# Optimization experiments

Measured on AMD Instinct MI355X. Metric: run time of the kernel, lower is better.

The kernel has to match this reference:

```python
import jax, jax.numpy as jnp
import numpy as np

TAU, LBDA, THETA = 0.25, 0.15, 0.3
N_WARPS, N_ITERS = 5, 5
EPS = 1e-12  # GRAD_IS_ZERO


def centered_gradient(x):
    # centered [-0.5,0,0.5] stencil with one-sided boundaries (matches conv+boundary-fix)
    dx = jnp.concatenate([0.5 * (x[..., 1:2] - x[..., 0:1]),
                          0.5 * (x[..., 2:] - x[..., :-2]),
                          0.5 * (x[..., -1:] - x[..., -2:-1])], axis=-1)
    dy = jnp.concatenate([0.5 * (x[:, :, 1:2] - x[:, :, 0:1]),
                          0.5 * (x[:, :, 2:] - x[:, :, :-2]),
                          0.5 * (x[:, :, -1:] - x[:, :, -2:-1])], axis=2)
    return dx, dy


def forward_gradient(x):
    # [-1,1] forward difference, zero at last col/row (conv 'same' + zeroed last slice)
    dx = jnp.concatenate([x[..., 1:] - x[..., :-1], jnp.zeros_like(x[..., :1])], axis=-1)
    dy = jnp.concatenate([x[:, :, 1:] - x[:, :, :-1], jnp.zeros_like(x[:, :, :1])], axis=2)
    return dx, dy


def forward_divergence(px, py):
    # backward difference with zero left/top boundary; last entry = -p[-2]
    dx = jnp.concatenate([px[..., :1], px[..., 1:-1] - px[..., :-2], -px[..., -2:-1]], axis=-1)
    dy = jnp.concatenate([py[:, :, :1], py[:, :, 1:-1] - py[:, :, :-2], -py[:, :, -2:-1]], axis=2)
    return dx + dy


def warp_image(im, u, v):
    # bilinear warp by pixel flow (u,v); grid math mirrors the STN spatial_transformer:
    # normalized identity grid in [-1,1] plus flow*2/size, mapped back via (g+1)*size/2,
    # with indices clipped to the image (border behavior).
    B, C, H, W = im.shape
    dt = im.dtype
    gx = jnp.linspace(-1.0, 1.0, W, dtype=dt)[None, None, None, :]
    gy = jnp.linspace(-1.0, 1.0, H, dtype=dt)[None, None, :, None]
    x = (gx + u * (2.0 / W) + 1.0) * (W / 2.0)
    y = (gy + v * (2.0 / H) + 1.0) * (H / 2.0)
    x0 = jnp.floor(x).astype(jnp.int32)
    y0 = jnp.floor(y).astype(jnp.int32)
    x0i = jnp.clip(x0, 0, W - 1); x1i = jnp.clip(x0 + 1, 0, W - 1)
    y0i = jnp.clip(y0, 0, H - 1); y1i = jnp.clip(y0 + 1, 0, H - 1)
    x0f = x0i.astype(dt); x1f = x1i.astype(dt)
    y0f = y0i.astype(dt); y1f = y1i.astype(dt)
    flat = im.reshape(B, H * W)

    def gather(yi, xi):
        idx = (yi * W + xi).reshape(B, H * W)
        return jnp.take_along_axis(flat, idx, axis=1).reshape(B, C, H, W)

    Ia = gather(y0i, x0i); Ib = gather(y1i, x0i)
    Ic = gather(y0i, x1i); Id = gather(y1i, x1i)
    wa = (x1f - x) * (y1f - y); wb = (x1f - x) * (y - y0f)
    wc = (x - x0f) * (y1f - y); wd = (x - x0f) * (y - y0f)
    return wa * Ia + wb * Ib + wc * Ic + wd * Id


def tv_l1_scale(x1, x2, u1, u2):
    l_t = LBDA * THETA
    taut = TAU / THETA
    d2x, d2y = centered_gradient(x2)
    z = jnp.zeros_like(x1)
    p11, p12, p21, p22 = z, z, z, z
    rho = z
    for _ in range(N_WARPS):
        x2w = warp_image(x2, u1, u2)
        dxw = warp_image(d2x, u1, u2)
        dyw = warp_image(d2y, u1, u2)
        grad = dxw * dxw + dyw * dyw + EPS
        rho_c = x2w - dxw * u1 - dyw * u2 - x1
        for _ in range(N_ITERS):
            rho = rho_c + dxw * u1 + dyw * u2 + EPS
            m1 = rho < -l_t * grad
            m2 = rho > l_t * grad
            m3 = (~m1) & (~m2) & (grad > EPS)
            s = jnp.where(m1, l_t, jnp.where(m2, -l_t, jnp.where(m3, -rho / grad, 0.0)))
            v1 = s * dxw + u1
            v2 = s * dyw + u2
            u1 = v1 + THETA * forward_divergence(p11, p12)
            u2 = v2 + THETA * forward_divergence(p21, p22)
            u1x, u1y = forward_gradient(u1)
            u2x, u2y = forward_gradient(u2)
            n1 = 1.0 + taut * jnp.sqrt(u1x * u1x + u1y * u1y + EPS)
            n2 = 1.0 + taut * jnp.sqrt(u2x * u2x + u2y * u2y + EPS)
            p11 = (p11 + taut * u1x) / n1
            p12 = (p12 + taut * u1y) / n1
            p21 = (p21 + taut * u2x) / n2
            p22 = (p22 + taut * u2y) / n2
    return u1, u2, rho


def setup_inputs() -> dict:
    key = jax.random.key(0)
    k1, k2 = jax.random.split(key)
    B, H, W = 8, 480, 480
    x1 = jax.random.uniform(k1, (B, 1, H, W), dtype=jnp.float32)
    x2 = jax.random.uniform(k2, (B, 1, H, W), dtype=jnp.float32)
    u1 = jnp.zeros((B, 1, H, W), dtype=jnp.float32)
    u2 = jnp.zeros((B, 1, H, W), dtype=jnp.float32)
    return {"x1": x1, "x2": x2, "u1": u1, "u2": u2}


def reference(x1, x2, u1, u2):
    return tv_l1_scale(x1, x2, u1, u2)
```

## Files before the change

### kernel.cpp

```cpp
#include <hip/hip_runtime.h>

#pragma clang fp contract(off)


constexpr int B = 8, H = 480, W = 480;
constexpr int HW = H * W;
constexpr int N = B * HW;

constexpr float THETA = (float)0.3;
constexpr float L_T  = (float)(0.15 * 0.3);
constexpr float TAUT = (float)(0.25 / 0.3);
constexpr float EPSF = (float)1e-12;

#define RW 42
#define RH 40
#define HALO 5
#define TW 32
#define TH 30
#define NTX 15
#define NTY 16
#define TPB 512
#define NPX 4
#define RPX (RW*RH)

template <int WARPK>
__global__ __launch_bounds__(TPB, 4) void k_fused(
    const float* __restrict__ x1, const float* __restrict__ x2,
    const float* __restrict__ u1In, const float* __restrict__ u2In,
    const float2* __restrict__ uIn, const float4* __restrict__ pIn,
    float* __restrict__ u1Out, float* __restrict__ u2Out,
    float2* __restrict__ uOut, float4* __restrict__ pOut,
    float* __restrict__ rhoOut)
{
  __shared__ float2 su[RPX];
  __shared__ float2 spA[RPX];
  __shared__ float2 spB[RPX];

  int blk = blockIdx.x;
  int bx = blk % NTX;
  int by = (blk / NTX) % NTY;
  int b  = blk / (NTX * NTY);
  const int ox = bx * TW - HALO;
  const int oy = by * TH - HALO;
  const int tid = threadIdx.x;
  const int base = b * HW;
  const float* __restrict__ im = x2 + base;

  float cdx[NPX], cdy[NPX], crc[NPX];

#pragma unroll
  for (int k = 0; k < NPX; ++k) {
    int idx = tid + k * TPB;
    if (idx < RPX) {
      int ly = idx / RW, lx = idx - ly * RW;
      int px = ox + lx, py = oy + ly;
      bool valid = (px >= 0 && px < W && py >= 0 && py < H);
      if (valid) {
        int gi = base + py * W + px;
        float u, v;
        if (WARPK == 0) { u = u1In[gi]; v = u2In[gi]; }
        else            { float2 uv = uIn[gi]; u = uv.x; v = uv.y; }
        const float step = 2.0f / 479.0f;
        float gx = -1.0f + (float)px * step;
        float gy = -1.0f + (float)py * step;
        float X = ((gx + u * (float)(2.0 / 480.0)) + 1.0f) * 240.0f;
        float Y = ((gy + v * (float)(2.0 / 480.0)) + 1.0f) * 240.0f;
        float fX = floorf(X), fY = floorf(Y);
        int ix = (int)fX, iy = (int)fY;
        int x0i = min(max(ix, 0), W - 1);
        int x1i = min(max(ix + 1, 0), W - 1);
        int y0i = min(max(iy, 0), H - 1);
        int y1i = min(max(iy + 1, 0), H - 1);
        float x0f = (float)x0i, x1f = (float)x1i;
        float y0f = (float)y0i, y1f = (float)y1i;
        float wa = (x1f - X) * (y1f - Y);
        float wb = (x1f - X) * (Y - y0f);
        float wc = (X - x0f) * (y1f - Y);
        float wd = (X - x0f) * (Y - y0f);
        int xmA = max(x0i - 1, 0), xpA = min(x0i + 1, W - 1);
        int xmB = max(x1i - 1, 0), xpB = min(x1i + 1, W - 1);
        int ymA = max(y0i - 1, 0), ypA = min(y0i + 1, H - 1);
        int ymB = max(y1i - 1, 0), ypB = min(y1i + 1, H - 1);
        int y0W = y0i * W, y1W = y1i * W;
        int ymAW = ymA * W, ypAW = ypA * W, ymBW = ymB * W, ypBW = ypB * W;
        float Ia = im[y0W + x0i], Ib = im[y1W + x0i];
        float Ic = im[y0W + x1i], Id = im[y1W + x1i];
        float dA = 0.5f * (im[y0W + xpA] - im[y0W + xmA]);
        float dB = 0.5f * (im[y1W + xpA] - im[y1W + xmA]);
        float dC = 0.5f * (im[y0W + xpB] - im[y0W + xmB]);
        float dD = 0.5f * (im[y1W + xpB] - im[y1W + xmB]);
        float eA = 0.5f * (im[ypAW + x0i] - im[ymAW + x0i]);
        float eB = 0.5f * (im[ypBW + x0i] - im[ymBW + x0i]);
        float eC = 0.5f * (im[ypAW + x1i] - im[ymAW + x1i]);
        float eD = 0.5f * (im[ypBW + x1i] - im[ymBW + x1i]);
        float x2w = ((wa * Ia + wb * Ib) + wc * Ic) + wd * Id;
        float dxw = ((wa * dA + wb * dB) + wc * dC) + wd * dD;
        float dyw = ((wa * eA + wb * eB) + wc * eC) + wd * eD;
        cdx[k] = dxw; cdy[k] = dyw;
        crc[k] = ((x2w - dxw * u) - dyw * v) - x1[gi];
        float4 q;
        if (WARPK == 0) q = make_float4(0.f, 0.f, 0.f, 0.f);
        else            q = pIn[gi];
        su[idx]  = make_float2(u, v);
        spA[idx] = make_float2(q.x, q.z);
        spB[idx] = make_float2(q.y, q.w);
      }
    }
  }
  __syncthreads();

  for (int t = 1; t <= 5; ++t) {
    int ulox = ox + t; if (ulox < 0) ulox = 0;
    int uloy = oy + t; if (uloy < 0) uloy = 0;
    int uhix = (ox + RW >= W) ? W : (ox + RW + 1 - t);
    int uhiy = (oy + RH >= H) ? H : (oy + RH + 1 - t);

#pragma unroll
    for (int k = 0; k < NPX; ++k) {
      int idx = tid + k * TPB;
      if (idx < RPX) {
        int ly = idx / RW, lx = idx - ly * RW;
        int px = ox + lx, py = oy + ly;
        if (px >= ulox && px < uhix && py >= uloy && py < uhiy) {
          float2 uo  = su[idx];
          float2 pAo = spA[idx];
          float2 pBo = spB[idx];
          float2 pl = spA[idx - 1];
          float2 pu = spB[idx - RW];
          float dx = cdx[k], dy = cdy[k];
          float u = uo.x, v = uo.y;
          float rho = ((crc[k] + dx * u) + dy * v) + EPSF;
          float grad = (dx * dx + dy * dy) + EPSF;
          float lt_g = L_T * grad;
          float s;
          if (rho < -lt_g)      s = L_T;
          else if (rho > lt_g)  s = -L_T;
          else if (grad > EPSF) s = (-rho) / grad;
          else                  s = 0.f;
          float v1 = s * dx + u;
          float v2 = s * dy + v;
          float dvx1, dvy1, dvx2, dvy2;
          if (px == 0)          dvx1 = pAo.x;
          else if (px == W - 1) dvx1 = -pl.x;
          else                  dvx1 = pAo.x - pl.x;
          if (py == 0)          dvy1 = pBo.x;
          else if (py == H - 1) dvy1 = -pu.x;
          else                  dvy1 = pBo.x - pu.x;
          if (px == 0)          dvx2 = pAo.y;
          else if (px == W - 1) dvx2 = -pl.y;
          else                  dvx2 = pAo.y - pl.y;
          if (py == 0)          dvy2 = pBo.y;
          else if (py == H - 1) dvy2 = -pu.y;
          else                  dvy2 = pBo.y - pu.y;
          float nu1 = v1 + THETA * (dvx1 + dvy1);
          float nu2 = v2 + THETA * (dvx2 + dvy2);
          su[idx] = make_float2(nu1, nu2);
          if (WARPK == 2 && t == 5) {
            if (lx >= HALO && lx < HALO + TW && ly >= HALO && ly < HALO + TH)
              rhoOut[base + py * W + px] = rho;
          }
        }
      }
    }
    __syncthreads();

    if (!(WARPK == 2 && t == 5)) {
      int phix = (ox + RW >= W) ? W : (ox + RW - t);
      int phiy = (oy + RH >= H) ? H : (oy + RH - t);
#pragma unroll
      for (int k = 0; k < NPX; ++k) {
        int idx = tid + k * TPB;
        if (idx < RPX) {
          int ly = idx / RW, lx = idx - ly * RW;
          int px = ox + lx, py = oy + ly;
          if (px >= ulox && px < phix && py >= uloy && py < phiy) {
            float2 uo = su[idx];
            float2 uR = su[idx + 1];
            float2 uD = su[idx + RW];
            float2 pAo = spA[idx];
            float2 pBo = spB[idx];
            float u1c = uo.x, u2c = uo.y;
            float u1x = (px < W - 1) ? uR.x - u1c : 0.f;
            float u1y = (py < H - 1) ? uD.x - u1c : 0.f;
            float u2x = (px < W - 1) ? uR.y - u2c : 0.f;
            float u2y = (py < H - 1) ? uD.y - u2c : 0.f;
            float n1 = 1.0f + TAUT * sqrtf((u1x * u1x + u1y * u1y) + EPSF);
            float n2 = 1.0f + TAUT * sqrtf((u2x * u2x + u2y * u2y) + EPSF);
            float np11 = (pAo.x + TAUT * u1x) / n1;
            float np12 = (pBo.x + TAUT * u1y) / n1;
            float np21 = (pAo.y + TAUT * u2x) / n2;
            float np22 = (pBo.y + TAUT * u2y) / n2;
            spA[idx] = make_float2(np11, np21);
            spB[idx] = make_float2(np12, np22);
          }
        }
      }
    }
    __syncthreads();
  }

#pragma unroll
  for (int k = 0; k < NPX; ++k) {
    int idx = tid + k * TPB;
    if (idx < RPX) {
      int ly = idx / RW, lx = idx - ly * RW;
      if (lx >= HALO && lx < HALO + TW && ly >= HALO && ly < HALO + TH) {
        int gi = base + (oy + ly) * W + (ox + lx);
        float2 uo = su[idx];
        if (WARPK == 2) {
          u1Out[gi] = uo.x;
          u2Out[gi] = uo.y;
        } else {
          uOut[gi] = uo;
          float2 a = spA[idx], c = spB[idx];
          pOut[gi] = make_float4(a.x, c.x, a.y, c.y);
        }
      }
    }
  }
}

extern "C" void kernel_launch(void* const* d_in, const int* in_sizes, int n_in,
                              void* d_out, int out_size, void* d_ws, size_t ws_size,
                              hipStream_t stream) {
  const float* x1 = (const float*)d_in[0];
  const float* x2 = (const float*)d_in[1];
  const float* u1_in = (const float*)d_in[2];
  const float* u2_in = (const float*)d_in[3];

  float* u1o  = (float*)d_out;
  float* u2o  = u1o + (size_t)N;
  float* rhoo = u1o + (size_t)2 * N;

  float* ws  = (float*)d_ws;
  float2* uA = (float2*)ws;
  float4* pA = (float4*)(ws + (size_t)2 * N);
  float2* uB = (float2*)(ws + (size_t)6 * N);
  float4* pB = (float4*)(ws + (size_t)8 * N);

  dim3 grd(NTX * NTY * B), blk(TPB);
  k_fused<0><<<grd, blk, 0, stream>>>(x1, x2, u1_in, u2_in, nullptr, nullptr,
                                      nullptr, nullptr, uA, pA, rhoo);
  k_fused<1><<<grd, blk, 0, stream>>>(x1, x2, nullptr, nullptr, uA, pA,
                                      nullptr, nullptr, uB, pB, rhoo);
  k_fused<1><<<grd, blk, 0, stream>>>(x1, x2, nullptr, nullptr, uB, pB,
                                      nullptr, nullptr, uA, pA, rhoo);
  k_fused<1><<<grd, blk, 0, stream>>>(x1, x2, nullptr, nullptr, uA, pA,
                                      nullptr, nullptr, uB, pB, rhoo);
  k_fused<2><<<grd, blk, 0, stream>>>(x1, x2, nullptr, nullptr, uB, pB,
                                      u1o, u2o, nullptr, nullptr, rhoo);
}
```

Baseline: 367.4 us.

## Keep per-pixel state in registers with vertical strips per thread and wider tiles

Each thread now owns a vertical strip of four pixels in one column and keeps u, p, and the warp coefficients in registers across the five inner iterations. Shared memory is used only for neighbours across strip boundaries, which cuts LDS traffic and drops the per-pixel index divisions. Per-pixel iteration limits are precomputed, and the precomputed grad and lambda*grad values are cached. The tile grows from 32 to 40 columns, which lowers the halo recompute ratio but raises register pressure and leaves 12 of 512 threads idle.

```diff
diff --git a/kernel.cpp b/kernel.cpp
--- a/kernel.cpp
+++ b/kernel.cpp
@@ -12,16 +12,16 @@
 constexpr float TAUT = (float)(0.25 / 0.3);
 constexpr float EPSF = (float)1e-12;
 
-#define RW 42
+#define RW 50
 #define RH 40
 #define HALO 5
-#define TW 32
+#define TW 40
 #define TH 30
-#define NTX 15
+#define NTX 12
 #define NTY 16
 #define TPB 512
-#define NPX 4
-#define RPX (RW*RH)
+#define NSTRIP 500
+#define SJ 4
 
 template <int WARPK>
 __global__ __launch_bounds__(TPB, 4) void k_fused(
@@ -32,188 +32,192 @@
     float2* __restrict__ uOut, float4* __restrict__ pOut,
     float* __restrict__ rhoOut)
 {
-  __shared__ float2 su[RPX];
-  __shared__ float2 spA[RPX];
-  __shared__ float2 spB[RPX];
-
-  int blk = blockIdx.x;
-  int bx = blk % NTX;
-  int by = (blk / NTX) % NTY;
-  int b  = blk / (NTX * NTY);
+  __shared__ float2 su[RW * RH];
+  __shared__ float2 spA[RW * RH];
+  __shared__ float2 spB[RW * RH];
+
+  const int blk = blockIdx.x;
+  const int bx = blk % NTX;
+  const int by = (blk / NTX) % NTY;
+  const int b  = blk / (NTX * NTY);
   const int ox = bx * TW - HALO;
   const int oy = by * TH - HALO;
   const int tid = threadIdx.x;
+  const bool ok = (tid < NSTRIP);
+  const int c  = tid % RW;
+  const int rs = tid / RW;
+  const int pxc = ox + c;
+  const int pyb = oy + rs * SJ;
+  const int idxb = rs * SJ * RW + c;
+  const bool bL = (pxc == 0), bR = (pxc == W - 1);
   const int base = b * HW;
   const float* __restrict__ im = x2 + base;
 
-  float cdx[NPX], cdy[NPX], crc[NPX];
-
-#pragma unroll
-  for (int k = 0; k < NPX; ++k) {
-    int idx = tid + k * TPB;
-    if (idx < RPX) {
-      int ly = idx / RW, lx = idx - ly * RW;
-      int px = ox + lx, py = oy + ly;
-      bool valid = (px >= 0 && px < W && py >= 0 && py < H);
-      if (valid) {
-        int gi = base + py * W + px;
-        float u, v;
-        if (WARPK == 0) { u = u1In[gi]; v = u2In[gi]; }
-        else            { float2 uv = uIn[gi]; u = uv.x; v = uv.y; }
-        const float step = 2.0f / 479.0f;
-        float gx = -1.0f + (float)px * step;
-        float gy = -1.0f + (float)py * step;
-        float X = ((gx + u * (float)(2.0 / 480.0)) + 1.0f) * 240.0f;
-        float Y = ((gy + v * (float)(2.0 / 480.0)) + 1.0f) * 240.0f;
-        float fX = floorf(X), fY = floorf(Y);
-        int ix = (int)fX, iy = (int)fY;
-        int x0i = min(max(ix, 0), W - 1);
-        int x1i = min(max(ix + 1, 0), W - 1);
-        int y0i = min(max(iy, 0), H - 1);
-        int y1i = min(max(iy + 1, 0), H - 1);
-        float x0f = (float)x0i, x1f = (float)x1i;
-        float y0f = (float)y0i, y1f = (float)y1i;
-        float wa = (x1f - X) * (y1f - Y);
-        float wb = (x1f - X) * (Y - y0f);
-        float wc = (X - x0f) * (y1f - Y);
-        float wd = (X - x0f) * (Y - y0f);
-        int xmA = max(x0i - 1, 0), xpA = min(x0i + 1, W - 1);
-        int xmB = max(x1i - 1, 0), xpB = min(x1i + 1, W - 1);
-        int ymA = max(y0i - 1, 0), ypA = min(y0i + 1, H - 1);
-        int ymB = max(y1i - 1, 0), ypB = min(y1i + 1, H - 1);
-        int y0W = y0i * W, y1W = y1i * W;
-        int ymAW = ymA * W, ypAW = ypA * W, ymBW = ymB * W, ypBW = ypB * W;
-        float Ia = im[y0W + x0i], Ib = im[y1W + x0i];
-        float Ic = im[y0W + x1i], Id = im[y1W + x1i];
-        float dA = 0.5f * (im[y0W + xpA] - im[y0W + xmA]);
-        float dB = 0.5f * (im[y1W + xpA] - im[y1W + xmA]);
-        float dC = 0.5f * (im[y0W + xpB] - im[y0W + xmB]);
-        float dD = 0.5f * (im[y1W + xpB] - im[y1W + xmB]);
-        float eA = 0.5f * (im[ypAW + x0i] - im[ymAW + x0i]);
-        float eB = 0.5f * (im[ypBW + x0i] - im[ymBW + x0i]);
-        float eC = 0.5f * (im[ypAW + x1i] - im[ymAW + x1i]);
-        float eD = 0.5f * (im[ypBW + x1i] - im[ymBW + x1i]);
-        float x2w = ((wa * Ia + wb * Ib) + wc * Ic) + wd * Id;
-        float dxw = ((wa * dA + wb * dB) + wc * dC) + wd * dD;
-        float dyw = ((wa * eA + wb * eB) + wc * eC) + wd * eD;
-        cdx[k] = dxw; cdy[k] = dyw;
-        crc[k] = ((x2w - dxw * u) - dyw * v) - x1[gi];
-        float4 q;
-        if (WARPK == 0) q = make_float4(0.f, 0.f, 0.f, 0.f);
-        else            q = pIn[gi];
-        su[idx]  = make_float2(u, v);
-        spA[idx] = make_float2(q.x, q.z);
-        spB[idx] = make_float2(q.y, q.w);
-      }
+  float ru1[SJ], ru2[SJ];
+  float rp11[SJ], rp12[SJ], rp21[SJ], rp22[SJ];
+  float cdx[SJ], cdy[SJ], crc[SJ];
+  float grd[SJ], ltg[SJ];
+  int   tu[SJ], tp[SJ];
+
+#pragma unroll
+  for (int j = 0; j < SJ; ++j) {
+    const int py = pyb + j;
+    const bool valid = ok && (pxc >= 0) && (pxc < W) && (py >= 0) && (py < H);
+    if (valid) {
+      int Lx = max(pxc - ox, -ox);
+      int Ly = max(py - oy, -oy);
+      int Rxu = (ox + RW >= W) ? 99 : (ox + RW - pxc);
+      int Ryu = (oy + RH >= H) ? 99 : (oy + RH - py);
+      tu[j] = min(min(Lx, Ly), min(Rxu, Ryu));
+      int Rxp = (ox + RW >= W) ? 99 : (ox + RW - 1 - pxc);
+      int Ryp = (oy + RH >= H) ? 99 : (oy + RH - 1 - py);
+      tp[j] = min(min(Lx, Ly), min(Rxp, Ryp));
+    } else { tu[j] = 0; tp[j] = 0; }
+    if (valid) {
+      const int gi = base + py * W + pxc;
+      float u, v;
+      if (WARPK == 0) { u = u1In[gi]; v = u2In[gi]; }
+      else            { float2 uv = uIn[gi]; u = uv.x; v = uv.y; }
+      const float step = 2.0f / 479.0f;
+      float gx = -1.0f + (float)pxc * step;
+      float gy = -1.0f + (float)py * step;
+      float X = ((gx + u * (float)(2.0 / 480.0)) + 1.0f) * 240.0f;
+      float Y = ((gy + v * (float)(2.0 / 480.0)) + 1.0f) * 240.0f;
+      float fX = floorf(X), fY = floorf(Y);
+      int ix = (int)fX, iy = (int)fY;
+      int x0i = min(max(ix, 0), W - 1);
+      int x1i = min(max(ix + 1, 0), W - 1);
+      int y0i = min(max(iy, 0), H - 1);
+      int y1i = min(max(iy + 1, 0), H - 1);
+      float x0f = (float)x0i, x1f = (float)x1i;
+      float y0f = (float)y0i, y1f = (float)y1i;
+      float wa = (x1f - X) * (y1f - Y);
+      float wb = (x1f - X) * (Y - y0f);
+      float wc = (X - x0f) * (y1f - Y);
+      float wd = (X - x0f) * (Y - y0f);
+      int xmA = max(x0i - 1, 0), xpA = min(x0i + 1, W - 1);
+      int xmB = max(x1i - 1, 0), xpB = min(x1i + 1, W - 1);
+      int ymA = max(y0i - 1, 0), ypA = min(y0i + 1, H - 1);
+      int ymB = max(y1i - 1, 0), ypB = min(y1i + 1, H - 1);
+      int y0W = y0i * W, y1W = y1i * W;
+      int ymAW = ymA * W, ypAW = ypA * W, ymBW = ymB * W, ypBW = ypB * W;
+      float Ia = im[y0W + x0i], Ib = im[y1W + x0i];
+      float Ic = im[y0W + x1i], Id = im[y1W + x1i];
+      float dA = 0.5f * (im[y0W + xpA] - im[y0W + xmA]);
+      float dB = 0.5f * (im[y1W + xpA] - im[y1W + xmA]);
+      float dC = 0.5f * (im[y0W + xpB] - im[y0W + xmB]);
+      float dD = 0.5f * (im[y1W + xpB] - im[y1W + xmB]);
+      float eA = 0.5f * (im[ypAW + x0i] - im[ymAW + x0i]);
+      float eB = 0.5f * (im[ypBW + x0i] - im[ymBW + x0i]);
+      float eC = 0.5f * (im[ypAW + x1i] - im[ymAW + x1i]);
+      float eD = 0.5f * (im[ypBW + x1i] - im[ymBW + x1i]);
+      float x2w = ((wa * Ia + wb * Ib) + wc * Ic) + wd * Id;
+      float dxw = ((wa * dA + wb * dB) + wc * dC) + wd * dD;
+      float dyw = ((wa * eA + wb * eB) + wc * eC) + wd * eD;
+      cdx[j] = dxw; cdy[j] = dyw;
+      crc[j] = ((x2w - dxw * u) - dyw * v) - x1[gi];
+      grd[j] = (dxw * dxw + dyw * dyw) + EPSF;
+      ltg[j] = L_T * grd[j];
+      ru1[j] = u; ru2[j] = v;
+      float4 q;
+      if (WARPK == 0) q = make_float4(0.f, 0.f, 0.f, 0.f);
+      else            q = pIn[gi];
+      rp11[j] = q.x; rp12[j] = q.y; rp21[j] = q.z; rp22[j] = q.w;
+      const int idx = idxb + j * RW;
+      spA[idx] = make_float2(q.x, q.z);
+      spB[idx] = make_float2(q.y, q.w);
     }
   }
   __syncthreads();
 
   for (int t = 1; t <= 5; ++t) {
-    int ulox = ox + t; if (ulox < 0) ulox = 0;
-    int uloy = oy + t; if (uloy < 0) uloy = 0;
-    int uhix = (ox + RW >= W) ? W : (ox + RW + 1 - t);
-    int uhiy = (oy + RH >= H) ? H : (oy + RH + 1 - t);
-
-#pragma unroll
-    for (int k = 0; k < NPX; ++k) {
-      int idx = tid + k * TPB;
-      if (idx < RPX) {
-        int ly = idx / RW, lx = idx - ly * RW;
-        int px = ox + lx, py = oy + ly;
-        if (px >= ulox && px < uhix && py >= uloy && py < uhiy) {
-          float2 uo  = su[idx];
-          float2 pAo = spA[idx];
-          float2 pBo = spB[idx];
-          float2 pl = spA[idx - 1];
-          float2 pu = spB[idx - RW];
-          float dx = cdx[k], dy = cdy[k];
-          float u = uo.x, v = uo.y;
-          float rho = ((crc[k] + dx * u) + dy * v) + EPSF;
-          float grad = (dx * dx + dy * dy) + EPSF;
-          float lt_g = L_T * grad;
-          float s;
-          if (rho < -lt_g)      s = L_T;
-          else if (rho > lt_g)  s = -L_T;
-          else if (grad > EPSF) s = (-rho) / grad;
-          else                  s = 0.f;
-          float v1 = s * dx + u;
-          float v2 = s * dy + v;
-          float dvx1, dvy1, dvx2, dvy2;
-          if (px == 0)          dvx1 = pAo.x;
-          else if (px == W - 1) dvx1 = -pl.x;
-          else                  dvx1 = pAo.x - pl.x;
-          if (py == 0)          dvy1 = pBo.x;
-          else if (py == H - 1) dvy1 = -pu.x;
-          else                  dvy1 = pBo.x - pu.x;
-          if (px == 0)          dvx2 = pAo.y;
-          else if (px == W - 1) dvx2 = -pl.y;
-          else                  dvx2 = pAo.y - pl.y;
-          if (py == 0)          dvy2 = pBo.y;
-          else if (py == H - 1) dvy2 = -pu.y;
-          else                  dvy2 = pBo.y - pu.y;
-          float nu1 = v1 + THETA * (dvx1 + dvy1);
-          float nu2 = v2 + THETA * (dvx2 + dvy2);
-          su[idx] = make_float2(nu1, nu2);
-          if (WARPK == 2 && t == 5) {
-            if (lx >= HALO && lx < HALO + TW && ly >= HALO && ly < HALO + TH)
-              rhoOut[base + py * W + px] = rho;
-          }
+#pragma unroll
+    for (int j = 0; j < SJ; ++j) {
+      if (t <= tu[j]) {
+        const int idx = idxb + j * RW;
+        const int py = pyb + j;
+        float dx = cdx[j], dy = cdy[j];
+        float u = ru1[j], v = ru2[j];
+        float rho = ((crc[j] + dx * u) + dy * v) + EPSF;
+        float s;
+        if (rho < -ltg[j])      s = L_T;
+        else if (rho > ltg[j])  s = -L_T;
+        else if (grd[j] > EPSF) s = (-rho) / grd[j];
+        else                    s = 0.f;
+        float v1 = s * dx + u;
+        float v2 = s * dy + v;
+        float2 pl = spA[idx - 1];
+        float pu12, pu22;
+        if (j == 0) { float2 q = spB[idx - RW]; pu12 = q.x; pu22 = q.y; }
+        else        { pu12 = rp12[j - 1];       pu22 = rp22[j - 1]; }
+        float dvx1, dvy1, dvx2, dvy2;
+        if (bL)               dvx1 = rp11[j];
+        else if (bR)          dvx1 = -pl.x;
+        else                  dvx1 = rp11[j] - pl.x;
+        if (py == 0)          dvy1 = rp12[j];
+        else if (py == H - 1) dvy1 = -pu12;
+        else                  dvy1 = rp12[j] - pu12;
+        if (bL)               dvx2 = rp21[j];
+        else if (bR)          dvx2 = -pl.y;
+        else                  dvx2 = rp21[j] - pl.y;
+        if (py == 0)          dvy2 = rp22[j];
+        else if (py == H - 1) dvy2 = -pu22;
+        else                  dvy2 = rp22[j] - pu22;
+        float nu1 = v1 + THETA * (dvx1 + dvy1);
+        float nu2 = v2 + THETA * (dvx2 + dvy2);
+        ru1[j] = nu1; ru2[j] = nu2;
+        if (!(WARPK == 2 && t == 5)) su[idx] = make_float2(nu1, nu2);
+        if (WARPK == 2 && t == 5) {
+          int ly = rs * SJ + j;
+          if (c >= HALO && c < HALO + TW && ly >= HALO && ly < HALO + TH)
+            rhoOut[base + py * W + pxc] = rho;
         }
       }
     }
     __syncthreads();
 
     if (!(WARPK == 2 && t == 5)) {
-      int phix = (ox + RW >= W) ? W : (ox + RW - t);
-      int phiy = (oy + RH >= H) ? H : (oy + RH - t);
-#pragma unroll
-      for (int k = 0; k < NPX; ++k) {
-        int idx = tid + k * TPB;
-        if (idx < RPX) {
-          int ly = idx / RW, lx = idx - ly * RW;
-          int px = ox + lx, py = oy + ly;
-          if (px >= ulox && px < phix && py >= uloy && py < phiy) {
-            float2 uo = su[idx];
-            float2 uR = su[idx + 1];
-            float2 uD = su[idx + RW];
-            float2 pAo = spA[idx];
-            float2 pBo = spB[idx];
-            float u1c = uo.x, u2c = uo.y;
-            float u1x = (px < W - 1) ? uR.x - u1c : 0.f;
-            float u1y = (py < H - 1) ? uD.x - u1c : 0.f;
-            float u2x = (px < W - 1) ? uR.y - u2c : 0.f;
-            float u2y = (py < H - 1) ? uD.y - u2c : 0.f;
-            float n1 = 1.0f + TAUT * sqrtf((u1x * u1x + u1y * u1y) + EPSF);
-            float n2 = 1.0f + TAUT * sqrtf((u2x * u2x + u2y * u2y) + EPSF);
-            float np11 = (pAo.x + TAUT * u1x) / n1;
-            float np12 = (pBo.x + TAUT * u1y) / n1;
-            float np21 = (pAo.y + TAUT * u2x) / n2;
-            float np22 = (pBo.y + TAUT * u2y) / n2;
-            spA[idx] = make_float2(np11, np21);
-            spB[idx] = make_float2(np12, np22);
-          }
+#pragma unroll
+      for (int j = 0; j < SJ; ++j) {
+        if (t <= tp[j]) {
+          const int idx = idxb + j * RW;
+          const int py = pyb + j;
+          float u1c = ru1[j], u2c = ru2[j];
+          float2 uR = su[idx + 1];
+          float uD1, uD2;
+          if (j < SJ - 1) { uD1 = ru1[j + 1]; uD2 = ru2[j + 1]; }
+          else            { float2 q = su[idx + RW]; uD1 = q.x; uD2 = q.y; }
+          float u1x = (pxc < W - 1) ? uR.x - u1c : 0.f;
+          float u1y = (py  < H - 1) ? uD1  - u1c : 0.f;
+          float u2x = (pxc < W - 1) ? uR.y - u2c : 0.f;
+          float u2y = (py  < H - 1) ? uD2  - u2c : 0.f;
+          float n1 = 1.0f + TAUT * sqrtf((u1x * u1x + u1y * u1y) + EPSF);
+          float n2 = 1.0f + TAUT * sqrtf((u2x * u2x + u2y * u2y) + EPSF);
+          float np11 = (rp11[j] + TAUT * u1x) / n1;
+          float np12 = (rp12[j] + TAUT * u1y) / n1;
+          float np21 = (rp21[j] + TAUT * u2x) / n2;
+          float np22 = (rp22[j] + TAUT * u2y) / n2;
+          rp11[j] = np11; rp12[j] = np12; rp21[j] = np21; rp22[j] = np22;
+          spA[idx] = make_float2(np11, np21);
+          if (j == SJ - 1) spB[idx] = make_float2(np12, np22);
         }
       }
-    }
-    __syncthreads();
+      __syncthreads();
+    }
   }
 
-#pragma unroll
-  for (int k = 0; k < NPX; ++k) {
-    int idx = tid + k * TPB;
-    if (idx < RPX) {
-      int ly = idx / RW, lx = idx - ly * RW;
-      if (lx >= HALO && lx < HALO + TW && ly >= HALO && ly < HALO + TH) {
-        int gi = base + (oy + ly) * W + (ox + lx);
-        float2 uo = su[idx];
+  if (ok && c >= HALO && c < HALO + TW) {
+#pragma unroll
+    for (int j = 0; j < SJ; ++j) {
+      int ly = rs * SJ + j;
+      if (ly >= HALO && ly < HALO + TH) {
+        int gi = base + (pyb + j) * W + pxc;
         if (WARPK == 2) {
-          u1Out[gi] = uo.x;
-          u2Out[gi] = uo.y;
+          u1Out[gi] = ru1[j];
+          u2Out[gi] = ru2[j];
         } else {
-          uOut[gi] = uo;
-          float2 a = spA[idx], c = spB[idx];
-          pOut[gi] = make_float4(a.x, c.x, a.y, c.y);
+          uOut[gi] = make_float2(ru1[j], ru2[j]);
+          pOut[gi] = make_float4(rp11[j], rp12[j], rp21[j], rp22[j]);
         }
       }
     }
```

New measurement: 373.9 us. Within noise of the previous version (+1.8%).

## Widen spatial tiles and hoist per-pixel iteration bounds into registers

Applied to the files above, without the earlier changes.

Widens the tile from 32 to 40 columns, so the 5-pixel halo is a smaller share of each block's work while the same 4 pixels-per-thread slots are kept. Each pixel's index math, the number of valid u/p update steps, the output mask, and the grad and lambda-theta-grad terms are computed once before the iteration loop, so the loop no longer recomputes bounds each step. It also removes the trailing barriers after the last step. The cost is more live registers under a 512x4 launch bound, and more shared memory per block, which may cut the number of resident blocks.

```diff
diff --git a/kernel.cpp b/kernel.cpp
--- a/kernel.cpp
+++ b/kernel.cpp
@@ -12,12 +12,12 @@
 constexpr float TAUT = (float)(0.25 / 0.3);
 constexpr float EPSF = (float)1e-12;
 
-#define RW 42
+#define RW 50
 #define RH 40
 #define HALO 5
-#define TW 32
+#define TW 40
 #define TH 30
-#define NTX 15
+#define NTX 12
 #define NTY 16
 #define TPB 512
 #define NPX 4
@@ -36,10 +36,10 @@
   __shared__ float2 spA[RPX];
   __shared__ float2 spB[RPX];
 
-  int blk = blockIdx.x;
-  int bx = blk % NTX;
-  int by = (blk / NTX) % NTY;
-  int b  = blk / (NTX * NTY);
+  const int blk = blockIdx.x;
+  const int bx = blk % NTX;
+  const int by = (blk / NTX) % NTY;
+  const int b  = blk / (NTX * NTY);
   const int ox = bx * TW - HALO;
   const int oy = by * TH - HALO;
   const int tid = threadIdx.x;
@@ -47,174 +47,171 @@
   const float* __restrict__ im = x2 + base;
 
   float cdx[NPX], cdy[NPX], crc[NPX];
+  float grd[NPX], ltg[NPX];
+  int   idxA[NPX], pxA[NPX], pyA[NPX], giA[NPX];
+  int   tu[NPX], tp[NPX];
+  bool  wout[NPX];
 
 #pragma unroll
   for (int k = 0; k < NPX; ++k) {
-    int idx = tid + k * TPB;
-    if (idx < RPX) {
-      int ly = idx / RW, lx = idx - ly * RW;
-      int px = ox + lx, py = oy + ly;
-      bool valid = (px >= 0 && px < W && py >= 0 && py < H);
-      if (valid) {
-        int gi = base + py * W + px;
-        float u, v;
-        if (WARPK == 0) { u = u1In[gi]; v = u2In[gi]; }
-        else            { float2 uv = uIn[gi]; u = uv.x; v = uv.y; }
-        const float step = 2.0f / 479.0f;
-        float gx = -1.0f + (float)px * step;
-        float gy = -1.0f + (float)py * step;
-        float X = ((gx + u * (float)(2.0 / 480.0)) + 1.0f) * 240.0f;
-        float Y = ((gy + v * (float)(2.0 / 480.0)) + 1.0f) * 240.0f;
-        float fX = floorf(X), fY = floorf(Y);
-        int ix = (int)fX, iy = (int)fY;
-        int x0i = min(max(ix, 0), W - 1);
-        int x1i = min(max(ix + 1, 0), W - 1);
-        int y0i = min(max(iy, 0), H - 1);
-        int y1i = min(max(iy + 1, 0), H - 1);
-        float x0f = (float)x0i, x1f = (float)x1i;
-        float y0f = (float)y0i, y1f = (float)y1i;
-        float wa = (x1f - X) * (y1f - Y);
-        float wb = (x1f - X) * (Y - y0f);
-        float wc = (X - x0f) * (y1f - Y);
-        float wd = (X - x0f) * (Y - y0f);
-        int xmA = max(x0i - 1, 0), xpA = min(x0i + 1, W - 1);
-        int xmB = max(x1i - 1, 0), xpB = min(x1i + 1, W - 1);
-        int ymA = max(y0i - 1, 0), ypA = min(y0i + 1, H - 1);
-        int ymB = max(y1i - 1, 0), ypB = min(y1i + 1, H - 1);
-        int y0W = y0i * W, y1W = y1i * W;
-        int ymAW = ymA * W, ypAW = ypA * W, ymBW = ymB * W, ypBW = ypB * W;
-        float Ia = im[y0W + x0i], Ib = im[y1W + x0i];
-        float Ic = im[y0W + x1i], Id = im[y1W + x1i];
-        float dA = 0.5f * (im[y0W + xpA] - im[y0W + xmA]);
-        float dB = 0.5f * (im[y1W + xpA] - im[y1W + xmA]);
-        float dC = 0.5f * (im[y0W + xpB] - im[y0W + xmB]);
-        float dD = 0.5f * (im[y1W + xpB] - im[y1W + xmB]);
-        float eA = 0.5f * (im[ypAW + x0i] - im[ymAW + x0i]);
-        float eB = 0.5f * (im[ypBW + x0i] - im[ymBW + x0i]);
-        float eC = 0.5f * (im[ypAW + x1i] - im[ymAW + x1i]);
-        float eD = 0.5f * (im[ypBW + x1i] - im[ymBW + x1i]);
-        float x2w = ((wa * Ia + wb * Ib) + wc * Ic) + wd * Id;
-        float dxw = ((wa * dA + wb * dB) + wc * dC) + wd * dD;
-        float dyw = ((wa * eA + wb * eB) + wc * eC) + wd * eD;
-        cdx[k] = dxw; cdy[k] = dyw;
-        crc[k] = ((x2w - dxw * u) - dyw * v) - x1[gi];
-        float4 q;
-        if (WARPK == 0) q = make_float4(0.f, 0.f, 0.f, 0.f);
-        else            q = pIn[gi];
-        su[idx]  = make_float2(u, v);
-        spA[idx] = make_float2(q.x, q.z);
-        spB[idx] = make_float2(q.y, q.w);
+    const int idx = tid + k * TPB;
+    idxA[k] = idx;
+    const int ly = idx / RW, lx = idx - ly * RW;
+    const int px = ox + lx, py = oy + ly;
+    pxA[k] = px; pyA[k] = py;
+    giA[k] = base + py * W + px;
+    const bool inreg = (idx < RPX);
+    const bool valid = inreg && (px >= 0) && (px < W) && (py >= 0) && (py < H);
+    wout[k] = inreg && lx >= HALO && lx < HALO + TW &&
+              ly >= HALO && ly < HALO + TH;
+    if (valid) {
+      int Lx = max(px - ox, -ox);
+      int Ly = max(py - oy, -oy);
+      int Rxu = (ox + RW >= W) ? 99 : (ox + RW - px);
+      int Ryu = (oy + RH >= H) ? 99 : (oy + RH - py);
+      tu[k] = min(min(Lx, Ly), min(Rxu, Ryu));
+      int Rxp = (ox + RW >= W) ? 99 : (ox + RW - 1 - px);
+      int Ryp = (oy + RH >= H) ? 99 : (oy + RH - 1 - py);
+      tp[k] = min(min(Lx, Ly), min(Rxp, Ryp));
+
+      const int gi = giA[k];
+      float u, v;
+      if (WARPK == 0) { u = u1In[gi]; v = u2In[gi]; }
+      else            { float2 uv = uIn[gi]; u = uv.x; v = uv.y; }
+      const float step = 2.0f / 479.0f;
+      float gx = -1.0f + (float)px * step;
+      float gy = -1.0f + (float)py * step;
+      float X = ((gx + u * (float)(2.0 / 480.0)) + 1.0f) * 240.0f;
+      float Y = ((gy + v * (float)(2.0 / 480.0)) + 1.0f) * 240.0f;
+      float fX = floorf(X), fY = floorf(Y);
+      int ix = (int)fX, iy = (int)fY;
+      int x0i = min(max(ix, 0), W - 1);
+      int x1i = min(max(ix + 1, 0), W - 1);
+      int y0i = min(max(iy, 0), H - 1);
+      int y1i = min(max(iy + 1, 0), H - 1);
+      float x0f = (float)x0i, x1f = (float)x1i;
+      float y0f = (float)y0i, y1f = (float)y1i;
+      float wa = (x1f - X) * (y1f - Y);
+      float wb = (x1f - X) * (Y - y0f);
+      float wc = (X - x0f) * (y1f - Y);
+      float wd = (X - x0f) * (Y - y0f);
+      int xmA = max(x0i - 1, 0), xpA = min(x0i + 1, W - 1);
+      int xmB = max(x1i - 1, 0), xpB = min(x1i + 1, W - 1);
+      int ymA = max(y0i - 1, 0), ypA = min(y0i + 1, H - 1);
+      int ymB = max(y1i - 1, 0), ypB = min(y1i + 1, H - 1);
+      int y0W = y0i * W, y1W = y1i * W;
+      int ymAW = ymA * W, ypAW = ypA * W, ymBW = ymB * W, ypBW = ypB * W;
+      float Ia = im[y0W + x0i], Ib = im[y1W + x0i];
+      float Ic = im[y0W + x1i], Id = im[y1W + x1i];
+      float dA = 0.5f * (im[y0W + xpA] - im[y0W + xmA]);
+      float dB = 0.5f * (im[y1W + xpA] - im[y1W + xmA]);
+      float dC = 0.5f * (im[y0W + xpB] - im[y0W + xmB]);
+      float dD = 0.5f * (im[y1W + xpB] - im[y1W + xmB]);
+      float eA = 0.5f * (im[ypAW + x0i] - im[ymAW + x0i]);
+      float eB = 0.5f * (im[ypBW + x0i] - im[ymBW + x0i]);
+      float eC = 0.5f * (im[ypAW + x1i] - im[ymAW + x1i]);
+      float eD = 0.5f * (im[ypBW + x1i] - im[ymBW + x1i]);
+      float x2w = ((wa * Ia + wb * Ib) + wc * Ic) + wd * Id;
+      float dxw = ((wa * dA + wb * dB) + wc * dC) + wd * dD;
+      float dyw = ((wa * eA + wb * eB) + wc * eC) + wd * eD;
+      cdx[k] = dxw; cdy[k] = dyw;
+      crc[k] = ((x2w - dxw * u) - dyw * v) - x1[gi];
+      grd[k] = (dxw * dxw + dyw * dyw) + EPSF;
+      ltg[k] = L_T * grd[k];
+      float4 q;
+      if (WARPK == 0) q = make_float4(0.f, 0.f, 0.f, 0.f);
+      else            q = pIn[gi];
+      su[idx]  = make_float2(u, v);
+      spA[idx] = make_float2(q.x, q.z);
+      spB[idx] = make_float2(q.y, q.w);
+    } else { tu[k] = 0; tp[k] = 0; }
+  }
+  __syncthreads();
+
+  for (int t = 1; t <= 5; ++t) {
+#pragma unroll
+    for (int k = 0; k < NPX; ++k) {
+      if (t <= tu[k]) {
+        const int idx = idxA[k];
+        float2 uo  = su[idx];
+        float2 pAo = spA[idx];
+        float2 pBo = spB[idx];
+        float2 pl = spA[idx - 1];
+        float2 pu = spB[idx - RW];
+        float dx = cdx[k], dy = cdy[k];
+        float u = uo.x, v = uo.y;
+        float rho = ((crc[k] + dx * u) + dy * v) + EPSF;
+        float s;
+        if (rho < -ltg[k])      s = L_T;
+        else if (rho > ltg[k])  s = -L_T;
+        else if (grd[k] > EPSF) s = (-rho) / grd[k];
+        else                    s = 0.f;
+        float v1 = s * dx + u;
+        float v2 = s * dy + v;
+        const int px = pxA[k], py = pyA[k];
+        float dvx1, dvy1, dvx2, dvy2;
+        if (px == 0)          dvx1 = pAo.x;
+        else if (px == W - 1) dvx1 = -pl.x;
+        else                  dvx1 = pAo.x - pl.x;
+        if (py == 0)          dvy1 = pBo.x;
+        else if (py == H - 1) dvy1 = -pu.x;
+        else                  dvy1 = pBo.x - pu.x;
+        if (px == 0)          dvx2 = pAo.y;
+        else if (px == W - 1) dvx2 = -pl.y;
+        else                  dvx2 = pAo.y - pl.y;
+        if (py == 0)          dvy2 = pBo.y;
+        else if (py == H - 1) dvy2 = -pu.y;
+        else                  dvy2 = pBo.y - pu.y;
+        float nu1 = v1 + THETA * (dvx1 + dvy1);
+        float nu2 = v2 + THETA * (dvx2 + dvy2);
+        su[idx] = make_float2(nu1, nu2);
+        if (WARPK == 2 && t == 5 && wout[k])
+          rhoOut[giA[k]] = rho;
       }
     }
-  }
-  __syncthreads();
-
-  for (int t = 1; t <= 5; ++t) {
-    int ulox = ox + t; if (ulox < 0) ulox = 0;
-    int uloy = oy + t; if (uloy < 0) uloy = 0;
-    int uhix = (ox + RW >= W) ? W : (ox + RW + 1 - t);
-    int uhiy = (oy + RH >= H) ? H : (oy + RH + 1 - t);
+    if (WARPK == 2 && t == 5) break;
+    __syncthreads();
 
 #pragma unroll
     for (int k = 0; k < NPX; ++k) {
-      int idx = tid + k * TPB;
-      if (idx < RPX) {
-        int ly = idx / RW, lx = idx - ly * RW;
-        int px = ox + lx, py = oy + ly;
-        if (px >= ulox && px < uhix && py >= uloy && py < uhiy) {
-          float2 uo  = su[idx];
-          float2 pAo = spA[idx];
-          float2 pBo = spB[idx];
-          float2 pl = spA[idx - 1];
-          float2 pu = spB[idx - RW];
-          float dx = cdx[k], dy = cdy[k];
-          float u = uo.x, v = uo.y;
-          float rho = ((crc[k] + dx * u) + dy * v) + EPSF;
-          float grad = (dx * dx + dy * dy) + EPSF;
-          float lt_g = L_T * grad;
-          float s;
-          if (rho < -lt_g)      s = L_T;
-          else if (rho > lt_g)  s = -L_T;
-          else if (grad > EPSF) s = (-rho) / grad;
-          else                  s = 0.f;
-          float v1 = s * dx + u;
-          float v2 = s * dy + v;
-          float dvx1, dvy1, dvx2, dvy2;
-          if (px == 0)          dvx1 = pAo.x;
-          else if (px == W - 1) dvx1 = -pl.x;
-          else                  dvx1 = pAo.x - pl.x;
-          if (py == 0)          dvy1 = pBo.x;
-          else if (py == H - 1) dvy1 = -pu.x;
-          else                  dvy1 = pBo.x - pu.x;
-          if (px == 0)          dvx2 = pAo.y;
-          else if (px == W - 1) dvx2 = -pl.y;
-          else                  dvx2 = pAo.y - pl.y;
-          if (py == 0)          dvy2 = pBo.y;
-          else if (py == H - 1) dvy2 = -pu.y;
-          else                  dvy2 = pBo.y - pu.y;
-          float nu1 = v1 + THETA * (dvx1 + dvy1);
-          float nu2 = v2 + THETA * (dvx2 + dvy2);
-          su[idx] = make_float2(nu1, nu2);
-          if (WARPK == 2 && t == 5) {
-            if (lx >= HALO && lx < HALO + TW && ly >= HALO && ly < HALO + TH)
-              rhoOut[base + py * W + px] = rho;
-          }
-        }
+      if (t <= tp[k]) {
+        const int idx = idxA[k];
+        float2 uo = su[idx];
+        float2 uR = su[idx + 1];
+        float2 uD = su[idx + RW];
+        float2 pAo = spA[idx];
+        float2 pBo = spB[idx];
+        const int px = pxA[k], py = pyA[k];
+        float u1c = uo.x, u2c = uo.y;
+        float u1x = (px < W - 1) ? uR.x - u1c : 0.f;
+        float u1y = (py < H - 1) ? uD.x - u1c : 0.f;
+        float u2x = (px < W - 1) ? uR.y - u2c : 0.f;
+        float u2y = (py < H - 1) ? uD.y - u2c : 0.f;
+        float n1 = 1.0f + TAUT * sqrtf((u1x * u1x + u1y * u1y) + EPSF);
+        float n2 = 1.0f + TAUT * sqrtf((u2x * u2x + u2y * u2y) + EPSF);
+        float np11 = (pAo.x + TAUT * u1x) / n1;
+        float np12 = (pBo.x + TAUT * u1y) / n1;
+        float np21 = (pAo.y + TAUT * u2x) / n2;
+        float np22 = (pBo.y + TAUT * u2y) / n2;
+        spA[idx] = make_float2(np11, np21);
+        spB[idx] = make_float2(np12, np22);
       }
     }
-    __syncthreads();
-
-    if (!(WARPK == 2 && t == 5)) {
-      int phix = (ox + RW >= W) ? W : (ox + RW - t);
-      int phiy = (oy + RH >= H) ? H : (oy + RH - t);
-#pragma unroll
-      for (int k = 0; k < NPX; ++k) {
-        int idx = tid + k * TPB;
-        if (idx < RPX) {
-          int ly = idx / RW, lx = idx - ly * RW;
-          int px = ox + lx, py = oy + ly;
-          if (px >= ulox && px < phix && py >= uloy && py < phiy) {
-            float2 uo = su[idx];
-            float2 uR = su[idx + 1];
-            float2 uD = su[idx + RW];
-            float2 pAo = spA[idx];
-            float2 pBo = spB[idx];
-            float u1c = uo.x, u2c = uo.y;
-            float u1x = (px < W - 1) ? uR.x - u1c : 0.f;
-            float u1y = (py < H - 1) ? uD.x - u1c : 0.f;
-            float u2x = (px < W - 1) ? uR.y - u2c : 0.f;
-            float u2y = (py < H - 1) ? uD.y - u2c : 0.f;
-            float n1 = 1.0f + TAUT * sqrtf((u1x * u1x + u1y * u1y) + EPSF);
-            float n2 = 1.0f + TAUT * sqrtf((u2x * u2x + u2y * u2y) + EPSF);
-            float np11 = (pAo.x + TAUT * u1x) / n1;
-            float np12 = (pBo.x + TAUT * u1y) / n1;
-            float np21 = (pAo.y + TAUT * u2x) / n2;
-            float np22 = (pBo.y + TAUT * u2y) / n2;
-            spA[idx] = make_float2(np11, np21);
-            spB[idx] = make_float2(np12, np22);
-          }
-        }
-      }
-    }
-    __syncthreads();
+    if (t < 5) __syncthreads();
   }
 
 #pragma unroll
   for (int k = 0; k < NPX; ++k) {
-    int idx = tid + k * TPB;
-    if (idx < RPX) {
-      int ly = idx / RW, lx = idx - ly * RW;
-      if (lx >= HALO && lx < HALO + TW && ly >= HALO && ly < HALO + TH) {
-        int gi = base + (oy + ly) * W + (ox + lx);
-        float2 uo = su[idx];
-        if (WARPK == 2) {
-          u1Out[gi] = uo.x;
-          u2Out[gi] = uo.y;
-        } else {
-          uOut[gi] = uo;
-          float2 a = spA[idx], c = spB[idx];
-          pOut[gi] = make_float4(a.x, c.x, a.y, c.y);
-        }
+    if (wout[k]) {
+      const int gi = giA[k];
+      float2 uo = su[idxA[k]];
+      if (WARPK == 2) {
+        u1Out[gi] = uo.x;
+        u2Out[gi] = uo.y;
+      } else {
+        uOut[gi] = uo;
+        float2 a = spA[idxA[k]], c = spB[idxA[k]];
+        pOut[gi] = make_float4(a.x, c.x, a.y, c.y);
       }
     }
   }
```

New measurement: 354.6 us. 3.5% less time.
